# Performance work log

Measured on AMD Instinct MI355X. Metric: run time of the kernel, lower is better.

Reference implementation:

```python
import jax, jax.numpy as jnp
import numpy as np
from jax import lax

B, W, L, E, V, C, H, O = 16384, 5, 20, 50, 100000, 128, 4096, 50


def setup_inputs() -> dict:
    key = jax.random.key(0)
    ks = jax.random.split(key, 10)
    x = jax.random.randint(ks[0], (B, W), 1, V)
    word_id_to_chars_ids = jax.random.randint(ks[1], (V, L), 0, C)
    word_emb = jax.random.normal(ks[2], (V, E), dtype=jnp.float32) * 0.1
    word_emb = word_emb.at[0].set(0.0)  # padding_idx=0
    char_emb = jax.random.normal(ks[3], (C, E), dtype=jnp.float32) * 0.1
    char_emb = char_emb.at[0].set(0.0)  # padding_idx=0
    conv_w = jax.random.normal(ks[4], (E, E, 3), dtype=jnp.float32) * (1.0 / np.sqrt(E * 3))
    conv_b = jax.random.normal(ks[5], (E,), dtype=jnp.float32) * 0.01
    fc1_w = jax.random.normal(ks[6], (H, E * W), dtype=jnp.float32) * (1.0 / np.sqrt(E * W))
    fc1_b = jnp.zeros((H,), dtype=jnp.float32)
    fc2_w = jax.random.normal(ks[7], (O, H), dtype=jnp.float32) * (1.0 / np.sqrt(H))
    fc2_b = jnp.zeros((O,), dtype=jnp.float32)
    return {"x": x, "word_id_to_chars_ids": word_id_to_chars_ids,
            "word_emb": word_emb, "char_emb": char_emb,
            "conv_w": conv_w, "conv_b": conv_b,
            "fc1_w": fc1_w, "fc1_b": fc1_b, "fc2_w": fc2_w, "fc2_b": fc2_b}


def reference(x, word_id_to_chars_ids, word_emb, char_emb, conv_w, conv_b,
              fc1_w, fc1_b, fc2_w, fc2_b):
    # per-window char ids: [B, 5, L] -> char embeddings [B, 5, L, E]
    char_ids = word_id_to_chars_ids[x]
    ce = char_emb[char_ids]
    # conv1d over char positions: reshape to NCW = [B*5, E, L]
    ce = ce.reshape(B * W, L, E).transpose(0, 2, 1)
    conv = lax.conv_general_dilated(ce, conv_w, window_strides=(1,),
                                    padding=[(1, 1)],
                                    dimension_numbers=("NCH", "OIH", "NCH"))
    conv = conv + conv_b[None, :, None]
    # max-pool over char positions (kernel == L): [B*5, E] -> [B, 5, E]
    chars = jnp.max(conv, axis=2).reshape(B, W, E)
    words = word_emb[x]  # [B, 5, E]
    h = (words + chars).reshape(B, W * E)  # view(-1, 250)
    h = jnp.tanh(h @ fc1_w.T + fc1_b)
    logits = h @ fc2_w.T + fc2_b
    return jax.nn.softmax(logits, axis=1)
```

## Files before the change

### kernel.cpp

```cpp
#include <hip/hip_runtime.h>
#include <hip/hip_bf16.h>


typedef __attribute__((ext_vector_type(8))) short short8;
typedef __attribute__((ext_vector_type(4))) float float4v;

__device__ inline short bf16b(float f) {
    __hip_bfloat16 h = __float2bfloat16(f);
    return *reinterpret_cast<short*>(&h);
}
__device__ inline uint packbf2(float a, float b) {
    return (uint)(ushort)bf16b(a) | ((uint)(ushort)bf16b(b) << 16);
}
__device__ inline void gload_lds16(const void* g, void* l) {
    __builtin_amdgcn_global_load_lds(
        (const __attribute__((address_space(1))) unsigned int*)g,
        (__attribute__((address_space(3))) unsigned int*)l, 16, 0, 0);
}

__global__ __launch_bounds__(256) void prep_kernel(
    const float* __restrict__ fc1_w, const float* __restrict__ fc1_b,
    const float* __restrict__ fc2_w, const float* __restrict__ char_emb,
    const float* __restrict__ conv_w, short* __restrict__ wbf,
    short* __restrict__ w2bf, float* __restrict__ gt,
    __hip_bfloat16* __restrict__ ha)
{
    const int bid = blockIdx.x;
    if (bid < 4096) {
        int idx = bid * 256 + threadIdx.x;
        int n = idx >> 8, k = idx & 255;
        float v = (k < 250) ? fc1_w[n * 250 + k] : (k == 250 ? fc1_b[n] : 0.f);
        int CT = n >> 4, mm = n & 15;
        int ks = k >> 5, qq = (k >> 3) & 3, j = k & 7;
        wbf[((CT * 8 + ks) * 64 + qq * 16 + mm) * 8 + j] = bf16b(v);
    } else if (bid < 5120) {
        int idx = (bid - 4096) * 256 + threadIdx.x;
        int o = idx >> 12, k = idx & 4095;
        float v = (o < 50) ? fc2_w[idx] : 0.f;
        int Ot = o >> 4, mm = o & 15;
        int kst = k >> 5, qq = (k >> 3) & 3, j = k & 7;
        w2bf[((kst * 4 + Ot) * 64 + qq * 16 + mm) * 8 + j] = bf16b(v);
    } else if (bid < 5195) {
        int idx = (bid - 5120) * 256 + threadIdx.x;
        if (idx >= 19200) return;
        int c = idx / 150, rem = idx - c * 150;
        int kk = rem / 50, o = rem - kk * 50;
        const float* ce = char_emb + c * 50;
        const float* w  = conv_w + o * 150 + kk;
        float s = 0.f;
        #pragma unroll 10
        for (int i = 0; i < 50; ++i) s += ce[i] * w[i * 3];
        gt[c * 156 + kk * 52 + o] = s;
    } else {
        int idx = (bid - 5195) * 256 + threadIdx.x;
        int b = idx / 6, j = idx - b * 6;
        ha[b * 256 + 250 + j] = __float2bfloat16(j == 0 ? 1.f : 0.f);
    }
}

__global__ __launch_bounds__(512) void conv_kernel(
    const int* __restrict__ x, const int* __restrict__ wci,
    const float* __restrict__ word_emb, const float* __restrict__ conv_b,
    const float* __restrict__ gt, __hip_bfloat16* __restrict__ ha)
{
    __shared__ float Gs[19968];
    char* gsb = (char*)Gs;

    const int tid = threadIdx.x;
    const int gw0 = blockIdx.x * 128;

    #pragma unroll
    for (int t = 0; t < 39; ++t)
        Gs[t * 512 + tid] = gt[t * 512 + tid];
    __syncthreads();

    {
        const int word = tid >> 2, part = tid & 3;
        const int xid = x[gw0 + word];
        const int* crow = wci + (size_t)xid * 20 + part * 5;
        char* hole = gsb + word * 624;
        #pragma unroll
        for (int j = 0; j < 5; ++j) {
            const int p = part * 5 + j;
            const int off = (p < 8) ? 200 + p : (p < 16 ? 400 + p : 600 + p);
            hole[off] = (char)crow[j];
        }
        if (part == 0) *(int*)(hole + 620) = xid;
    }
    __syncthreads();

    const int lane = tid & 63;
    const int wv   = tid >> 6;
    const int oc   = (lane < 50) ? lane : 49;
    const int oc4  = oc * 4;
    const float cbias = conv_b[oc];

    for (int it = 0; it < 16; ++it) {
        const int wl = it * 8 + wv;
        const char* hb = gsb + wl * 624;
        const uint cw0 = *(const uint*)(hb + 200);
        const uint cw1 = *(const uint*)(hb + 204);
        const uint cw2 = *(const uint*)(hb + 408);
        const uint cw3 = *(const uint*)(hb + 412);
        const uint cw4 = *(const uint*)(hb + 616);
        const int xid  = *(const int*)(hb + 620);

        int cb[20];
        #pragma unroll
        for (int p = 0; p < 20; ++p) {
            const uint cwv = (p < 4) ? cw0 : (p < 8) ? cw1 : (p < 12) ? cw2
                           : (p < 16) ? cw3 : cw4;
            const int c = (int)((cwv >> ((p & 3) * 8)) & 0xFF);
            cb[p] = c * 624 + oc4;
        }

        float mx = *(const float*)(gsb + cb[0] + 208)
                 + *(const float*)(gsb + cb[1] + 416);
        #pragma unroll
        for (int l = 1; l < 19; ++l) {
            float s = *(const float*)(gsb + cb[l] + 208)
                    + *(const float*)(gsb + cb[l - 1])
                    + *(const float*)(gsb + cb[l + 1] + 416);
            mx = fmaxf(mx, s);
        }
        {
            float s = *(const float*)(gsb + cb[19] + 208)
                    + *(const float*)(gsb + cb[18]);
            mx = fmaxf(mx, s);
        }

        const float wer = word_emb[(size_t)xid * 50 + oc];
        const float res = mx + cbias + wer;
        const int gw = gw0 + wl;
        const int b = gw / 5, wp = gw - b * 5;
        if (lane < 50)
            ha[b * 256 + wp * 50 + lane] = __float2bfloat16(res);
    }
}

__global__ __launch_bounds__(512, 1) void fused_kernel(
    const __hip_bfloat16* __restrict__ ha, const short* __restrict__ wbf,
    const short* __restrict__ w2bf, float* __restrict__ gpart)
{
    __shared__ char smem[147456];
    short8* Bsv = (short8*)smem;
    char*   hsb = smem + 131072;
    float*  partf = (float*)smem;

    const int tid  = threadIdx.x;
    const int lane = tid & 63;
    const int wv   = tid >> 6;
    const int wr = wv >> 2, wc = wv & 3;
    const int q = lane >> 4, m = lane & 15;
    const int rg = blockIdx.x >> 1, kh = blockIdx.x & 1;
    const int m0 = rg * 64;
    const int q2base = q >> 1, slot = q & 1;

    const short8* wbfv  = (const short8*)wbf;
    const short8* w2bfv = (const short8*)w2bf;
    const short8* hav   = (const short8*)ha;

    short8 av[2][8];
    #pragma unroll
    for (int mt = 0; mt < 2; ++mt)
        #pragma unroll
        for (int ks = 0; ks < 8; ++ks)
            av[mt][ks] = hav[(size_t)(m0 + wr * 32 + mt * 16 + m) * 32 + ks * 4 + q];
    #pragma unroll
    for (int mt = 0; mt < 2; ++mt)
        #pragma unroll
        for (int ks = 0; ks < 8; ++ks)
            asm volatile("" : "+v"(av[mt][ks]));

    #pragma unroll
    for (int i = 0; i < 8; ++i)
        gload_lds16(wbfv + (size_t)(kh * 16) * 4096 + i * 512 + tid,
                    Bsv + i * 512 + tid);
    __syncthreads();

    float4v acc2[2][4] = {};

    #pragma unroll 4
    for (int chl = 0; chl < 16; ++chl) {
        const int buf = chl & 1;
        const int chg = kh * 16 + chl;

        short8 b2[4];
        #pragma unroll
        for (int Ot = 0; Ot < 4; ++Ot)
            b2[Ot] = w2bfv[(size_t)((chg * 4 + wc) * 4 + Ot) * 64 + lane];

        #pragma unroll
        for (int i = 0; i < 8; ++i)
            gload_lds16(wbfv + (size_t)(chg + 1) * 4096 + i * 512 + tid,
                        Bsv + (buf ^ 1) * 4096 + i * 512 + tid);

        float4v acc[2][2] = {};
        #pragma unroll
        for (int ks = 0; ks < 8; ++ks) {
            short8 bv[2];
            #pragma unroll
            for (int nt = 0; nt < 2; ++nt)
                bv[nt] = Bsv[buf * 4096 + ((wc * 2 + nt) * 8 + ks) * 64 + lane];
            #pragma unroll
            for (int mt = 0; mt < 2; ++mt)
                #pragma unroll
                for (int nt = 0; nt < 2; ++nt)
                    acc[mt][nt] = __builtin_amdgcn_mfma_f32_16x16x32_bf16(
                        bv[nt], av[mt][ks], acc[mt][nt], 0, 0, 0);
        }

        #pragma unroll
        for (int mt = 0; mt < 2; ++mt) {
            const int frag = (wr * 2 + mt) * 4 + wc;
            #pragma unroll
            for (int nt = 0; nt < 2; ++nt) {
                float tv[4];
                #pragma unroll
                for (int r = 0; r < 4; ++r)
                    tv[r] = 1.f - 2.f / (__expf(2.f * acc[mt][nt][r]) + 1.f);
                const int q2 = nt * 2 + q2base;
                const uint p0 = packbf2(tv[0], tv[1]);
                const uint p1 = packbf2(tv[2], tv[3]);
                *(uint2*)(hsb + ((frag * 64 + q2 * 16 + m) * 16 + slot * 8))
                    = make_uint2(p0, p1);
            }
        }

        {
            short8 a2[2];
            #pragma unroll
            for (int mt = 0; mt < 2; ++mt)
                a2[mt] = *(const short8*)(hsb
                    + (((wr * 2 + mt) * 4 + wc) * 64 + lane) * 16);
            #pragma unroll
            for (int mt = 0; mt < 2; ++mt)
                #pragma unroll
                for (int Ot = 0; Ot < 4; ++Ot)
                    acc2[mt][Ot] = __builtin_amdgcn_mfma_f32_16x16x32_bf16(
                        a2[mt], b2[Ot], acc2[mt][Ot], 0, 0, 0);
        }

        __syncthreads();
    }

    #pragma unroll
    for (int mt = 0; mt < 2; ++mt)
        #pragma unroll
        for (int Ot = 0; Ot < 4; ++Ot)
            #pragma unroll
            for (int r = 0; r < 4; ++r)
                partf[(size_t)wc * 4096
                      + ((wr * 2 + mt) * 16 + q * 4 + r) * 64 + Ot * 16 + m]
                    = acc2[mt][Ot][r];
    __syncthreads();

    #pragma unroll
    for (int t = 0; t < 8; ++t) {
        int idx = t * 512 + tid;
        float s = partf[idx] + partf[4096 + idx]
                + partf[8192 + idx] + partf[12288 + idx];
        gpart[(size_t)blockIdx.x * 4096 + idx] = s;
    }
}

__global__ __launch_bounds__(256) void combine_kernel(
    const float* __restrict__ gpart, const float* __restrict__ fc2_b,
    float* __restrict__ out)
{
    const int tid  = threadIdx.x;
    const int lane = tid & 63;
    const int wv   = tid >> 6;
    const float bias = (lane < 50) ? fc2_b[lane] : 0.f;

    #pragma unroll
    for (int rr = 0; rr < 8; ++rr) {
        const int row = blockIdx.x * 32 + wv * 8 + rr;
        const int rg = row >> 6, rl = row & 63;
        float v = gpart[(size_t)(rg * 2) * 4096 + rl * 64 + lane]
                + gpart[(size_t)(rg * 2 + 1) * 4096 + rl * 64 + lane];
        v = (lane < 50) ? v + bias : -1e30f;
        float mx = v;
        #pragma unroll
        for (int off = 32; off > 0; off >>= 1) mx = fmaxf(mx, __shfl_xor(mx, off));
        float e = __expf(v - mx);
        float s = e;
        #pragma unroll
        for (int off = 32; off > 0; off >>= 1) s += __shfl_xor(s, off);
        if (lane < 50)
            out[(size_t)row * 50 + lane] = e / s;
    }
}

extern "C" void kernel_launch(void* const* d_in, const int* in_sizes, int n_in,
                              void* d_out, int out_size, void* d_ws, size_t ws_size,
                              hipStream_t stream) {
    const int*   x        = (const int*)  d_in[0];
    const int*   wci      = (const int*)  d_in[1];
    const float* word_emb = (const float*)d_in[2];
    const float* char_emb = (const float*)d_in[3];
    const float* conv_w   = (const float*)d_in[4];
    const float* conv_b   = (const float*)d_in[5];
    const float* fc1_w    = (const float*)d_in[6];
    const float* fc1_b    = (const float*)d_in[7];
    const float* fc2_w    = (const float*)d_in[8];
    const float* fc2_b    = (const float*)d_in[9];
    float* out = (float*)d_out;

    char* ws = (char*)d_ws;
    __hip_bfloat16* ha  = (__hip_bfloat16*)ws;
    short* wbf   = (short*)(ws + ((size_t)8  << 20));
    short* w2bf  = (short*)(ws + ((size_t)10 << 20));
    float* gtp   = (float*)(ws + ((size_t)11 << 20));
    float* gpart = (float*)(ws + ((size_t)16 << 20));

    prep_kernel<<<5579, 256, 0, stream>>>(fc1_w, fc1_b, fc2_w, char_emb,
                                          conv_w, wbf, w2bf, gtp, ha);
    conv_kernel<<<640, 512, 0, stream>>>(x, wci, word_emb, conv_b, gtp, ha);
    fused_kernel<<<512, 512, 0, stream>>>(ha, wbf, w2bf, gpart);
    combine_kernel<<<512, 256, 0, stream>>>(gpart, fc2_b, out);
}
```

Before: 204.4 us.

## Read fc1 weights directly from global and drop LDS staging and barriers

The fused MLP kernel no longer double-buffers fc1 weight chunks into LDS with async global-to-LDS loads. Each wave now loads its B fragments straight from global memory and computes four N-tiles instead of two. Blocks shrink to 256 threads with 48KB of LDS so that two blocks can share a CU. Each wave's tanh staging region is now private to that wave, which removes the per-chunk __syncthreads. The trade is that weights are re-fetched through L2/L1 by every wave instead of being shared via LDS, and more accumulator registers are live per wave.

New measurement: 228.4 us. +11.8%, slower.

```diff
diff --git a/kernel.cpp b/kernel.cpp
--- a/kernel.cpp
+++ b/kernel.cpp
@@ -11,11 +11,6 @@
 }
 __device__ inline uint packbf2(float a, float b) {
     return (uint)(ushort)bf16b(a) | ((uint)(ushort)bf16b(b) << 16);
-}
-__device__ inline void gload_lds16(const void* g, void* l) {
-    __builtin_amdgcn_global_load_lds(
-        (const __attribute__((address_space(1))) unsigned int*)g,
-        (__attribute__((address_space(3))) unsigned int*)l, 16, 0, 0);
 }
 
 __global__ __launch_bounds__(256) void prep_kernel(
@@ -138,19 +133,18 @@
     }
 }
 
-__global__ __launch_bounds__(512, 1) void fused_kernel(
+__global__ __launch_bounds__(256, 2) void fused_kernel(
     const __hip_bfloat16* __restrict__ ha, const short* __restrict__ wbf,
     const short* __restrict__ w2bf, float* __restrict__ gpart)
 {
-    __shared__ char smem[147456];
-    short8* Bsv = (short8*)smem;
-    char*   hsb = smem + 131072;
-    float*  partf = (float*)smem;
+    __shared__ char smem[49152];
+    float* partf = (float*)smem;
+    char*  hsb   = smem + 32768;
 
     const int tid  = threadIdx.x;
     const int lane = tid & 63;
     const int wv   = tid >> 6;
-    const int wr = wv >> 2, wc = wv & 3;
+    const int wr = wv >> 1, wc2 = wv & 1;
     const int q = lane >> 4, m = lane & 15;
     const int rg = blockIdx.x >> 1, kh = blockIdx.x & 1;
     const int m0 = rg * 64;
@@ -172,54 +166,36 @@
         for (int ks = 0; ks < 8; ++ks)
             asm volatile("" : "+v"(av[mt][ks]));
 
-    #pragma unroll
-    for (int i = 0; i < 8; ++i)
-        gload_lds16(wbfv + (size_t)(kh * 16) * 4096 + i * 512 + tid,
-                    Bsv + i * 512 + tid);
-    __syncthreads();
-
     float4v acc2[2][4] = {};
 
-    #pragma unroll 4
     for (int chl = 0; chl < 16; ++chl) {
-        const int buf = chl & 1;
         const int chg = kh * 16 + chl;
 
-        short8 b2[4];
-        #pragma unroll
-        for (int Ot = 0; Ot < 4; ++Ot)
-            b2[Ot] = w2bfv[(size_t)((chg * 4 + wc) * 4 + Ot) * 64 + lane];
-
-        #pragma unroll
-        for (int i = 0; i < 8; ++i)
-            gload_lds16(wbfv + (size_t)(chg + 1) * 4096 + i * 512 + tid,
-                        Bsv + (buf ^ 1) * 4096 + i * 512 + tid);
-
-        float4v acc[2][2] = {};
+        float4v acc[2][4] = {};
         #pragma unroll
         for (int ks = 0; ks < 8; ++ks) {
-            short8 bv[2];
-            #pragma unroll
-            for (int nt = 0; nt < 2; ++nt)
-                bv[nt] = Bsv[buf * 4096 + ((wc * 2 + nt) * 8 + ks) * 64 + lane];
+            short8 bv[4];
+            #pragma unroll
+            for (int nt = 0; nt < 4; ++nt)
+                bv[nt] = wbfv[(size_t)((chg * 8 + wc2 * 4 + nt) * 8 + ks) * 64 + lane];
             #pragma unroll
             for (int mt = 0; mt < 2; ++mt)
                 #pragma unroll
-                for (int nt = 0; nt < 2; ++nt)
+                for (int nt = 0; nt < 4; ++nt)
                     acc[mt][nt] = __builtin_amdgcn_mfma_f32_16x16x32_bf16(
                         bv[nt], av[mt][ks], acc[mt][nt], 0, 0, 0);
         }
 
         #pragma unroll
         for (int mt = 0; mt < 2; ++mt) {
-            const int frag = (wr * 2 + mt) * 4 + wc;
-            #pragma unroll
-            for (int nt = 0; nt < 2; ++nt) {
+            #pragma unroll
+            for (int nt = 0; nt < 4; ++nt) {
                 float tv[4];
                 #pragma unroll
                 for (int r = 0; r < 4; ++r)
                     tv[r] = 1.f - 2.f / (__expf(2.f * acc[mt][nt][r]) + 1.f);
-                const int q2 = nt * 2 + q2base;
+                const int frag = (wr * 2 + mt) * 4 + wc2 * 2 + (nt >> 1);
+                const int q2 = (nt & 1) * 2 + q2base;
                 const uint p0 = packbf2(tv[0], tv[1]);
                 const uint p1 = packbf2(tv[2], tv[3]);
                 *(uint2*)(hsb + ((frag * 64 + q2 * 16 + m) * 16 + slot * 8))
@@ -227,12 +203,17 @@
             }
         }
 
-        {
-            short8 a2[2];
+        #pragma unroll
+        for (int kf2 = 0; kf2 < 2; ++kf2) {
+            const int kf = wc2 * 2 + kf2;
+            short8 b2[4], a2[2];
+            #pragma unroll
+            for (int Ot = 0; Ot < 4; ++Ot)
+                b2[Ot] = w2bfv[(size_t)((chg * 4 + kf) * 4 + Ot) * 64 + lane];
             #pragma unroll
             for (int mt = 0; mt < 2; ++mt)
                 a2[mt] = *(const short8*)(hsb
-                    + (((wr * 2 + mt) * 4 + wc) * 64 + lane) * 16);
+                    + (((wr * 2 + mt) * 4 + kf) * 64 + lane) * 16);
             #pragma unroll
             for (int mt = 0; mt < 2; ++mt)
                 #pragma unroll
@@ -240,8 +221,6 @@
                     acc2[mt][Ot] = __builtin_amdgcn_mfma_f32_16x16x32_bf16(
                         a2[mt], b2[Ot], acc2[mt][Ot], 0, 0, 0);
         }
-
-        __syncthreads();
     }
 
     #pragma unroll
@@ -250,16 +229,15 @@
         for (int Ot = 0; Ot < 4; ++Ot)
             #pragma unroll
             for (int r = 0; r < 4; ++r)
-                partf[(size_t)wc * 4096
+                partf[(size_t)wc2 * 4096
                       + ((wr * 2 + mt) * 16 + q * 4 + r) * 64 + Ot * 16 + m]
                     = acc2[mt][Ot][r];
     __syncthreads();
 
     #pragma unroll
-    for (int t = 0; t < 8; ++t) {
-        int idx = t * 512 + tid;
-        float s = partf[idx] + partf[4096 + idx]
-                + partf[8192 + idx] + partf[12288 + idx];
+    for (int t = 0; t < 16; ++t) {
+        int idx = t * 256 + tid;
+        float s = partf[idx] + partf[4096 + idx];
         gpart[(size_t)blockIdx.x * 4096 + idx] = s;
     }
 }
@@ -317,6 +295,6 @@
     prep_kernel<<<5579, 256, 0, stream>>>(fc1_w, fc1_b, fc2_w, char_emb,
                                           conv_w, wbf, w2bf, gtp, ha);
     conv_kernel<<<640, 512, 0, stream>>>(x, wci, word_emb, conv_b, gtp, ha);
-    fused_kernel<<<512, 512, 0, stream>>>(ha, wbf, w2bf, gpart);
+    fused_kernel<<<512, 256, 0, stream>>>(ha, wbf, w2bf, gpart);
     combine_kernel<<<512, 256, 0, stream>>>(gpart, fc2_b, out);
 }
```
